# Optimization experiments

Hardware: AMD Instinct MI355X
Metric: run time of the kernel (lower is better)

The kernel has to match this reference:

```python
import jax, jax.numpy as jnp
import numpy as np

# config constants
B, S, H = 4, 2048, 1024
E = 8                 # n_routed_experts
M = 512               # moe_intermediate_size
K = 2                 # num_experts_per_tok
N_SHARED = 2
SM = M * N_SHARED     # shared expert intermediate
G = 64                # gene_size
GE_TEMP = 1.0
ALPHA = 0.001         # aux_loss_alpha
SEQ_AUX = True
NORM_TOPK = True
COS_TEMP = 0.78
CONS_ALPHA = 0.01
LEAKY_SLOPE = 0.01
EPS_COS = 1e-8


def setup_inputs() -> dict:
    key = jax.random.key(0)
    ks = jax.random.split(key, 12)
    sh = 1.0 / np.sqrt(H)
    sm = 1.0 / np.sqrt(M)
    ssm = 1.0 / np.sqrt(SM)
    sg = 1.0 / np.sqrt(G)
    return {
        "hidden_states": jax.random.normal(ks[0], (B, S, H), jnp.float32),
        "g": jax.random.normal(ks[1], (B, G), jnp.float32),
        "wt": jax.random.uniform(ks[2], (E, H), jnp.float32, -sh, sh),   # gate weight_token
        "wg": jax.random.uniform(ks[3], (E, G), jnp.float32, -sg, sg),   # gate weight_gene
        "w_gate": jax.random.uniform(ks[4], (E, H, M), jnp.float32, -sh, sh),
        "w_up": jax.random.uniform(ks[5], (E, H, M), jnp.float32, -sh, sh),
        "w_down": jax.random.uniform(ks[6], (E, M, H), jnp.float32, -sm, sm),
        "sw_gate": jax.random.uniform(ks[7], (H, SM), jnp.float32, -sh, sh),
        "sw_up": jax.random.uniform(ks[8], (H, SM), jnp.float32, -sh, sh),
        "sw_down": jax.random.uniform(ks[9], (SM, H), jnp.float32, -ssm, ssm),
    }


def _leaky(x):
    return jnp.where(x >= 0, x, LEAKY_SLOPE * x)


def _moe_forward(hidden_states, g, wt, wg, w_gate, w_up, w_down, sw_gate, sw_up, sw_down):
    b, s, h = hidden_states.shape
    x = hidden_states.reshape(-1, h)                    # [T, H], T = b*s
    T = x.shape[0]

    # ---- gate ----
    logits_h = x @ wt.T                                 # [T, E]
    logits_g = g @ wg.T                                 # [b, E]
    logits_g = jnp.repeat(logits_g, s, axis=0)          # [T, E]
    logits = (logits_h + logits_g / GE_TEMP) / (1.0 + 1.0 / GE_TEMP)
    scores = jax.nn.softmax(logits, axis=-1)            # [T, E]
    topk_w, topk_idx = jax.lax.top_k(scores, K)         # [T, K]
    if K > 1 and NORM_TOPK:
        topk_w = topk_w / (topk_w.sum(-1, keepdims=True) + 1e-20)

    # aux loss (seq_aux=True)
    onehot = jax.nn.one_hot(topk_idx.reshape(b, s * K), E, dtype=jnp.float32)  # [b, s*K, E]
    ce = onehot.sum(1) / (s * K / E)                    # [b, E]
    aux_loss = (ce * scores.reshape(b, s, E).mean(1)).sum(1).mean() * ALPHA

    # ---- routed experts: dense stacked compute, then gather ----
    gp = _leaky(jnp.einsum('th,ehm->etm', x, w_gate))   # [E, T, M]
    up = jnp.einsum('th,ehm->etm', x, w_up)
    y_all = jnp.einsum('etm,emh->eth', gp * up, w_down) # [E, T, H]
    y_sel = y_all[topk_idx, jnp.arange(T)[:, None], :]  # [T, K, H]
    y = (y_sel * topk_w[..., None]).sum(1).reshape(b, s, h)

    # ---- shared expert ----
    p = (_leaky(hidden_states @ sw_gate) * (hidden_states @ sw_up)) @ sw_down
    y = y + p

    # consistency cosine loss
    num = jnp.sum(y * p, -1)
    den = jnp.maximum(jnp.linalg.norm(y, axis=-1), EPS_COS) * jnp.maximum(jnp.linalg.norm(p, axis=-1), EPS_COS)
    closs = CONS_ALPHA * jnp.mean((num / den) / (1.0 + COS_TEMP))
    return y, aux_loss + closs


def reference(hidden_states, g, wt, wg, w_gate, w_up, w_down, sw_gate, sw_up, sw_down):
    y, _ = _moe_forward(hidden_states, g, wt, wg, w_gate, w_up, w_down, sw_gate, sw_up, sw_down)
    return y
```

## Files before the change

### kernel.cpp

```cpp
#include <hip/hip_runtime.h>
#include <stdint.h>

#define T_TOK 8192
#define H_DIM 1024
#define M_DIM 512
#define SM_DIM 1024
#define E_NUM 8
#define S_SEQ 2048
#define G_DIM 64
#define NASSIGN 16384
#define NSLOT (NASSIGN + E_NUM * 256)
#define MAX_TILES (NASSIGN / 256 + E_NUM)
#define NBLK_PLACE (NASSIGN / 256)

typedef float f32x4 __attribute__((ext_vector_type(4)));
typedef short bf16x8 __attribute__((ext_vector_type(8)));

struct TileDesc { int base; int expert; int nrows; };

#define WAITCNT_VM6 asm volatile("s_waitcnt vmcnt(6)" ::: "memory")
#define WAITCNT_VM4 asm volatile("s_waitcnt vmcnt(4)" ::: "memory")
#define WAITCNT_VM2 asm volatile("s_waitcnt vmcnt(2)" ::: "memory")
#define WAITCNT_VM0 asm volatile("s_waitcnt vmcnt(0)" ::: "memory")
#define WAITCNT_LGKM0 asm volatile("s_waitcnt lgkmcnt(0)" ::: "memory")

static __device__ __forceinline__ ushort f2b(float f) {
  union { float f; uint32_t u; } a; a.f = f;
  uint32_t r = a.u + 0x7fffu + ((a.u >> 16) & 1u);
  return (ushort)(r >> 16);
}
static __device__ __forceinline__ float b2f(ushort u) {
  union { uint32_t u; float f; } a; a.u = ((uint32_t)u) << 16;
  return a.f;
}
static __device__ __forceinline__ int imin(int a, int b) { return a < b ? a : b; }

static __device__ __forceinline__ void gll16(const void* g, void* l) {
  __builtin_amdgcn_global_load_lds(
      (const __attribute__((address_space(1))) void*)g,
      (__attribute__((address_space(3))) void*)l, 16, 0, 0);
}
static __device__ __forceinline__ int xcd_remap(int wg, int nwg) {
  return (wg & 7) * (nwg >> 3) + (wg >> 3);
}

__global__ void cvt_x_kernel(const float* __restrict__ x, ushort* __restrict__ xb) {
  int i = blockIdx.x * 256 + threadIdx.x;
  const float4 v = ((const float4*)x)[i];
  ushort4 o;
  o.x = f2b(v.x); o.y = f2b(v.y); o.z = f2b(v.z); o.w = f2b(v.w);
  ((ushort4*)xb)[i] = o;
}

__global__ void tcvt_kernel(const float* __restrict__ src, ushort* __restrict__ dst, int R, int C) {
  __shared__ float tile[32][33];
  size_t bo = (size_t)blockIdx.z * R * C;
  src += bo; dst += bo;
  int c0 = blockIdx.x * 32, r0 = blockIdx.y * 32;
#pragma unroll
  for (int i = 0; i < 4; ++i)
    tile[threadIdx.y + i * 8][threadIdx.x] =
        src[(size_t)(r0 + threadIdx.y + i * 8) * C + c0 + threadIdx.x];
  __syncthreads();
#pragma unroll
  for (int i = 0; i < 4; ++i)
    dst[(size_t)(c0 + threadIdx.y + i * 8) * R + r0 + threadIdx.x] =
        f2b(tile[threadIdx.x][threadIdx.y + i * 8]);
}

__global__ void lg_kernel(const float* __restrict__ g, const float* __restrict__ wg,
                          float* __restrict__ lg) {
  int tid = threadIdx.x;
  if (tid < 4 * E_NUM) {
    int b = tid >> 3, e = tid & 7;
    float s = 0.f;
    for (int i = 0; i < G_DIM; ++i) s += g[b * G_DIM + i] * wg[e * G_DIM + i];
    lg[tid] = s;
  }
}

__global__ __launch_bounds__(64) void router_kernel(
    const float* __restrict__ x, const float* __restrict__ wt, const float* __restrict__ lg,
    int* __restrict__ tidx, float* __restrict__ tw) {
  int t = blockIdx.x;
  int lane = threadIdx.x;
  const float* xr = x + (size_t)t * H_DIM;
  float a[E_NUM];
#pragma unroll
  for (int e = 0; e < E_NUM; ++e) a[e] = 0.f;
  for (int i = lane; i < H_DIM; i += 64) {
    float xv = xr[i];
#pragma unroll
    for (int e = 0; e < E_NUM; ++e) a[e] += xv * wt[e * H_DIM + i];
  }
#pragma unroll
  for (int e = 0; e < E_NUM; ++e)
    for (int off = 32; off; off >>= 1) a[e] += __shfl_xor(a[e], off, 64);
  if (lane == 0) {
    int b = t / S_SEQ;
    float l[E_NUM];
#pragma unroll
    for (int e = 0; e < E_NUM; ++e) l[e] = 0.5f * (a[e] + lg[b * E_NUM + e]);
    int i1 = 0; float b1 = l[0];
#pragma unroll
    for (int e = 1; e < E_NUM; ++e) if (l[e] > b1) { b1 = l[e]; i1 = e; }
    int i2 = -1; float b2 = -1e30f;
#pragma unroll
    for (int e = 0; e < E_NUM; ++e) if (e != i1 && l[e] > b2) { b2 = l[e]; i2 = e; }
    float e2 = expf(b2 - b1);
    float inv = 1.f / (1.f + e2);
    tidx[t * 2] = i1; tidx[t * 2 + 1] = i2;
    tw[t * 2] = inv;  tw[t * 2 + 1] = e2 * inv;
  }
}

__global__ __launch_bounds__(256) void hist_kernel(const int* __restrict__ tidx,
                                                   int* __restrict__ bcount) {
  __shared__ int h[E_NUM];
  int tid = threadIdx.x;
  if (tid < E_NUM) h[tid] = 0;
  __syncthreads();
  atomicAdd(&h[tidx[blockIdx.x * 256 + tid]], 1);
  __syncthreads();
  if (tid < E_NUM) bcount[blockIdx.x * E_NUM + tid] = h[tid];
}

__global__ __launch_bounds__(64) void scan2_kernel(
    const int* __restrict__ bcount, int* __restrict__ boffs, int* __restrict__ offs,
    TileDesc* __restrict__ desc, int* __restrict__ ndesc) {
  __shared__ int cnt[E_NUM];
  __shared__ int off_s[E_NUM];
  int lane = threadIdx.x;
  if (lane < E_NUM) {
    int s = 0;
    for (int b = 0; b < NBLK_PLACE; ++b) s += bcount[b * E_NUM + lane];
    cnt[lane] = s;
  }
  __syncthreads();
  if (lane == 0) {
    int o = 0, nd = 0;
    for (int e = 0; e < E_NUM; ++e) {
      off_s[e] = o;
      offs[e] = o;
      int n = cnt[e];
      for (int tb = 0; tb < n; tb += 256) {
        desc[nd].base = o + tb; desc[nd].expert = e;
        desc[nd].nrows = imin(n - tb, 256);
        ++nd;
      }
      o += n;
    }
    offs[E_NUM] = o;
    *ndesc = nd;
  }
  __syncthreads();
  if (lane < E_NUM) {
    int run = off_s[lane];
    for (int b = 0; b < NBLK_PLACE; ++b) {
      boffs[b * E_NUM + lane] = run;
      run += bcount[b * E_NUM + lane];
    }
  }
}

__global__ __launch_bounds__(256) void place2_kernel(
    const int* __restrict__ tidx, const int* __restrict__ boffs,
    int* __restrict__ perm, int* __restrict__ slot_of) {
  __shared__ int wcnt[4][E_NUM];
  int tid = threadIdx.x, wv = tid >> 6, lane = tid & 63;
  int i = blockIdx.x * 256 + tid;
  int e = tidx[i];
  unsigned long long lower = (lane == 63) ? 0x7fffffffffffffffull : ((1ull << lane) - 1ull);
  int rank = 0;
#pragma unroll
  for (int ee = 0; ee < E_NUM; ++ee) {
    unsigned long long m = __ballot(e == ee);
    if (e == ee) rank = __popcll(m & lower);
    if (lane == 0) wcnt[wv][ee] = __popcll(m);
  }
  __syncthreads();
  int off = boffs[blockIdx.x * E_NUM + e];
  for (int w = 0; w < wv; ++w) off += wcnt[w][e];
  int pos = off + rank;
  perm[pos] = i >> 1;
  slot_of[i] = pos;
}

template <int DUAL>
static __device__ __forceinline__ void gemm_core8(
    const ushort* __restrict__ A, const ushort* __restrict__ B0,
    const ushort* __restrict__ B1, void* __restrict__ Out, int outf32,
    int Kd, int NdOut, int rowbase, int nrows, int n0,
    const int* __restrict__ perm, ushort* __restrict__ LDS) {
  int tid = threadIdx.x, wv = tid >> 6, lane = tid & 63;
  int wr = wv >> 2, wc = wv & 3;
  int lr = lane & 15, cg = lane >> 4;
  int sid = lane >> 3, dch = lane & 7;

  const ushort* apA[2][2];
  const ushort* apB[2][2];
#pragma unroll
  for (int qm = 0; qm < 2; ++qm)
#pragma unroll
    for (int k = 0; k < 2; ++k) {
      int idx = k * 64 + wv * 8 + sid;
      int gch = dch ^ (idx & 7);
      int grow = (idx >> 6) * 128 + qm * 64 + (idx & 63);
      grow = imin(grow, nrows - 1);
      int arow = perm ? perm[rowbase + grow] : rowbase + grow;
      apA[qm][k] = A + (size_t)arow * Kd + gch * 8;
    }
#pragma unroll
  for (int qn = 0; qn < 2; ++qn)
#pragma unroll
    for (int k = 0; k < 2; ++k) {
      int idx = k * 64 + wv * 8 + sid;
      int gch = dch ^ (idx & 7);
      int vrow = n0 + (idx >> 5) * 64 + qn * 32 + (idx & 31);
      const ushort* src; int brow;
      if (DUAL) {
        src = ((vrow >> 4) & 1) ? B1 : B0;
        brow = (vrow >> 5) * 16 + (vrow & 15);
      } else {
        src = B0; brow = vrow;
      }
      apB[qn][k] = src + (size_t)brow * Kd + gch * 8;
    }

  auto stgA = [&](int qm, int k, int nd) {
    gll16(apA[qm][k], LDS + nd * 16384 + qm * 8192 + (k * 512 + wv * 64) * 8);
    apA[qm][k] += 64;
  };
  auto stgB = [&](int qn, int k, int nd) {
    gll16(apB[qn][k], LDS + 32768 + nd * 16384 + qn * 8192 + (k * 512 + wv * 64) * 8);
    apB[qn][k] += 64;
  };
  auto rdA = [&](int d, int qm, int m, int kk) -> bf16x8 {
    int idx = wr * 64 + m * 16 + lr;
    int ch = (kk * 4 + cg) ^ (idx & 7);
    return *(const bf16x8*)(LDS + d * 16384 + qm * 8192 + idx * 64 + ch * 8);
  };
  auto rdB = [&](int d, int qn, int n, int kk) -> bf16x8 {
    int idx = wc * 32 + n * 16 + lr;
    int ch = (kk * 4 + cg) ^ (idx & 7);
    return *(const bf16x8*)(LDS + 32768 + d * 16384 + qn * 8192 + idx * 64 + ch * 8);
  };

  f32x4 acc[2][2][4][2];
#pragma unroll
  for (int qm = 0; qm < 2; ++qm)
#pragma unroll
    for (int qn = 0; qn < 2; ++qn)
#pragma unroll
      for (int m = 0; m < 4; ++m)
#pragma unroll
        for (int n = 0; n < 2; ++n) acc[qm][qn][m][n] = (f32x4){0.f, 0.f, 0.f, 0.f};

  int nk = Kd >> 6;
  stgA(0, 0, 0); stgA(0, 1, 0);
  stgB(0, 0, 0); stgB(0, 1, 0);
  stgB(1, 0, 0); stgB(1, 1, 0);
  stgA(1, 0, 0); stgA(1, 1, 0);
  WAITCNT_VM4;
  __builtin_amdgcn_s_barrier();

  for (int t = 0; t < nk; ++t) {
    int cur = t & 1, nxt = cur ^ 1;
    bool hn = (t + 1 < nk);
    bf16x8 a0f[4][2], a1f[4][2], b0f[2][2], b1f[2][2];

#pragma unroll
    for (int m = 0; m < 4; ++m) { a0f[m][0] = rdA(cur, 0, m, 0); a0f[m][1] = rdA(cur, 0, m, 1); }
#pragma unroll
    for (int n = 0; n < 2; ++n) { b0f[n][0] = rdB(cur, 0, n, 0); b0f[n][1] = rdB(cur, 0, n, 1); }
    if (hn) { stgA(0, 0, nxt); stgA(0, 1, nxt); WAITCNT_VM4; } else { WAITCNT_VM2; }
    WAITCNT_LGKM0;
    __builtin_amdgcn_s_barrier();
    __builtin_amdgcn_s_setprio(1);
#pragma unroll
    for (int m = 0; m < 4; ++m)
#pragma unroll
      for (int n = 0; n < 2; ++n) {
        acc[0][0][m][n] = __builtin_amdgcn_mfma_f32_16x16x32_bf16(a0f[m][0], b0f[n][0], acc[0][0][m][n], 0, 0, 0);
        acc[0][0][m][n] = __builtin_amdgcn_mfma_f32_16x16x32_bf16(a0f[m][1], b0f[n][1], acc[0][0][m][n], 0, 0, 0);
      }
    __builtin_amdgcn_s_setprio(0);

#pragma unroll
    for (int n = 0; n < 2; ++n) { b1f[n][0] = rdB(cur, 1, n, 0); b1f[n][1] = rdB(cur, 1, n, 1); }
    if (hn) { stgB(0, 0, nxt); stgB(0, 1, nxt); WAITCNT_VM4; } else { WAITCNT_VM0; }
    WAITCNT_LGKM0;
    __builtin_amdgcn_s_barrier();
    __builtin_amdgcn_s_setprio(1);
#pragma unroll
    for (int m = 0; m < 4; ++m)
#pragma unroll
      for (int n = 0; n < 2; ++n) {
        acc[0][1][m][n] = __builtin_amdgcn_mfma_f32_16x16x32_bf16(a0f[m][0], b1f[n][0], acc[0][1][m][n], 0, 0, 0);
        acc[0][1][m][n] = __builtin_amdgcn_mfma_f32_16x16x32_bf16(a0f[m][1], b1f[n][1], acc[0][1][m][n], 0, 0, 0);
      }
    __builtin_amdgcn_s_setprio(0);

#pragma unroll
    for (int m = 0; m < 4; ++m) { a1f[m][0] = rdA(cur, 1, m, 0); a1f[m][1] = rdA(cur, 1, m, 1); }
    if (hn) { stgB(1, 0, nxt); stgB(1, 1, nxt); WAITCNT_VM6; }
    WAITCNT_LGKM0;
    __builtin_amdgcn_s_barrier();
    __builtin_amdgcn_s_setprio(1);
#pragma unroll
    for (int m = 0; m < 4; ++m)
#pragma unroll
      for (int n = 0; n < 2; ++n) {
        acc[1][0][m][n] = __builtin_amdgcn_mfma_f32_16x16x32_bf16(a1f[m][0], b0f[n][0], acc[1][0][m][n], 0, 0, 0);
        acc[1][0][m][n] = __builtin_amdgcn_mfma_f32_16x16x32_bf16(a1f[m][1], b0f[n][1], acc[1][0][m][n], 0, 0, 0);
      }
    __builtin_amdgcn_s_setprio(0);

    if (hn) { stgA(1, 0, nxt); stgA(1, 1, nxt); WAITCNT_VM4; }
    WAITCNT_LGKM0;
    __builtin_amdgcn_s_barrier();
    __builtin_amdgcn_s_setprio(1);
#pragma unroll
    for (int m = 0; m < 4; ++m)
#pragma unroll
      for (int n = 0; n < 2; ++n) {
        acc[1][1][m][n] = __builtin_amdgcn_mfma_f32_16x16x32_bf16(a1f[m][0], b1f[n][0], acc[1][1][m][n], 0, 0, 0);
        acc[1][1][m][n] = __builtin_amdgcn_mfma_f32_16x16x32_bf16(a1f[m][1], b1f[n][1], acc[1][1][m][n], 0, 0, 0);
      }
    __builtin_amdgcn_s_setprio(0);
  }

#pragma unroll
  for (int qm = 0; qm < 2; ++qm)
#pragma unroll
    for (int qn = 0; qn < 2; ++qn)
#pragma unroll
      for (int m = 0; m < 4; ++m)
#pragma unroll
        for (int r = 0; r < 4; ++r) {
          int row = wr * 128 + qm * 64 + m * 16 + cg * 4 + r;
          if (row < nrows) {
            if (DUAL) {
              float gv = acc[qm][qn][m][0][r], uv = acc[qm][qn][m][1][r];
              float hv = (gv >= 0.f ? gv : 0.01f * gv) * uv;
              int col = ((n0 >> 5) + wc * 2 + qn) * 16 + lr;
              ((ushort*)Out)[(size_t)(rowbase + row) * NdOut + col] = f2b(hv);
            } else {
#pragma unroll
              for (int n = 0; n < 2; ++n) {
                int col = n0 + wc * 64 + qn * 32 + n * 16 + lr;
                size_t o = (size_t)(rowbase + row) * NdOut + col;
                if (outf32) ((float*)Out)[o] = acc[qm][qn][m][n][r];
                else ((ushort*)Out)[o] = f2b(acc[qm][qn][m][n][r]);
              }
            }
          }
        }
}

__global__ __launch_bounds__(512) void gemm_dual_all(
    const ushort* __restrict__ xb, const ushort* __restrict__ swg,
    const ushort* __restrict__ swu, ushort* __restrict__ hsh,
    const ushort* __restrict__ wg, const ushort* __restrict__ wu,
    ushort* __restrict__ h_e, const int* __restrict__ perm,
    const TileDesc* __restrict__ desc, const int* __restrict__ ndesc) {
  __shared__ ushort LDS[65536];
  int id = xcd_remap(blockIdx.x, gridDim.x);
  if (id < 256) {
    int mt = id >> 3, n0 = (id & 7) * 256;
    gemm_core8<1>(xb, swg, swu, hsh, 0, H_DIM, SM_DIM, mt * 256, 256, n0, nullptr, LDS);
  } else {
    int rid = id - 256;
    int mt = rid >> 2, n0 = (rid & 3) * 256;
    if (mt >= *ndesc) return;
    TileDesc d = desc[mt];
    size_t wo = (size_t)d.expert * M_DIM * H_DIM;
    gemm_core8<1>(xb, wg + wo, wu + wo, h_e, 0, H_DIM, M_DIM, d.base, d.nrows, n0, perm, LDS);
  }
}

__global__ __launch_bounds__(512) void gemm_down_all(
    const ushort* __restrict__ hsh, const ushort* __restrict__ swd, float* __restrict__ y,
    const ushort* __restrict__ h_e, const ushort* __restrict__ wd, ushort* __restrict__ ye,
    const TileDesc* __restrict__ desc, const int* __restrict__ ndesc) {
  __shared__ ushort LDS[65536];
  int id = xcd_remap(blockIdx.x, gridDim.x);
  if (id < 128) {
    int mt = id >> 2, n0 = (id & 3) * 256;
    gemm_core8<0>(hsh, swd, nullptr, (void*)y, 1, SM_DIM, H_DIM, mt * 256, 256, n0, nullptr, LDS);
  } else {
    int rid = id - 128;
    int mt = rid >> 2, n0 = (rid & 3) * 256;
    if (mt >= *ndesc) return;
    TileDesc d = desc[mt];
    gemm_core8<0>(h_e, wd + (size_t)d.expert * H_DIM * M_DIM, nullptr, (void*)ye, 0,
                  M_DIM, H_DIM, d.base, d.nrows, n0, nullptr, LDS);
  }
}

__global__ void final_kernel(float* __restrict__ y, const ushort* __restrict__ ye,
                             const int* __restrict__ slot_of, const float* __restrict__ tw) {
  int i = blockIdx.x * 256 + threadIdx.x;
  int t = i >> 8;
  int c4 = (i & 255) * 4;
  int s0 = slot_of[t * 2], s1 = slot_of[t * 2 + 1];
  float w0 = tw[t * 2], w1 = tw[t * 2 + 1];
  float4 v = ((float4*)y)[i];
  ushort4 a = *(const ushort4*)(ye + (size_t)s0 * H_DIM + c4);
  ushort4 b = *(const ushort4*)(ye + (size_t)s1 * H_DIM + c4);
  v.x += w0 * b2f(a.x) + w1 * b2f(b.x);
  v.y += w0 * b2f(a.y) + w1 * b2f(b.y);
  v.z += w0 * b2f(a.z) + w1 * b2f(b.z);
  v.w += w0 * b2f(a.w) + w1 * b2f(b.w);
  ((float4*)y)[i] = v;
}

extern "C" void kernel_launch(void* const* d_in, const int* in_sizes, int n_in,
                              void* d_out, int out_size, void* d_ws, size_t ws_size,
                              hipStream_t stream) {
  const float* x       = (const float*)d_in[0];
  const float* g       = (const float*)d_in[1];
  const float* wt      = (const float*)d_in[2];
  const float* wg      = (const float*)d_in[3];
  const float* w_gate  = (const float*)d_in[4];
  const float* w_up    = (const float*)d_in[5];
  const float* w_down  = (const float*)d_in[6];
  const float* sw_gate = (const float*)d_in[7];
  const float* sw_up   = (const float*)d_in[8];
  const float* sw_down = (const float*)d_in[9];
  float* y = (float*)d_out;

  char* p = (char*)d_ws;
  auto alloc = [&](size_t bytes) -> char* {
    char* r = p;
    p += (bytes + 255) & ~(size_t)255;
    return r;
  };
  ushort* xb    = (ushort*)alloc((size_t)T_TOK * H_DIM * 2);
  ushort* wg_t  = (ushort*)alloc((size_t)E_NUM * M_DIM * H_DIM * 2);
  ushort* wu_t  = (ushort*)alloc((size_t)E_NUM * M_DIM * H_DIM * 2);
  ushort* wd_t  = (ushort*)alloc((size_t)E_NUM * H_DIM * M_DIM * 2);
  ushort* swg_t = (ushort*)alloc((size_t)SM_DIM * H_DIM * 2);
  ushort* swu_t = (ushort*)alloc((size_t)SM_DIM * H_DIM * 2);
  ushort* swd_t = (ushort*)alloc((size_t)H_DIM * SM_DIM * 2);
  float* lg     = (float*)alloc(4 * E_NUM * 4);
  int* tidx     = (int*)alloc(NASSIGN * 4);
  float* tw     = (float*)alloc(NASSIGN * 4);
  int* bcount   = (int*)alloc(NBLK_PLACE * E_NUM * 4);
  int* boffs    = (int*)alloc(NBLK_PLACE * E_NUM * 4);
  int* offs     = (int*)alloc((E_NUM + 1) * 4);
  int* ndesc    = (int*)alloc(4);
  int* perm     = (int*)alloc(NASSIGN * 4);
  int* slot_of  = (int*)alloc(NASSIGN * 4);
  TileDesc* desc = (TileDesc*)alloc(MAX_TILES * sizeof(TileDesc));
  ushort* h_e   = (ushort*)alloc((size_t)NSLOT * M_DIM * 2);
  ushort* hsh   = (ushort*)alloc((size_t)T_TOK * SM_DIM * 2);
  ushort* ye    = (ushort*)alloc((size_t)NSLOT * H_DIM * 2);
  (void)ws_size; (void)in_sizes; (void)n_in; (void)out_size;

  cvt_x_kernel<<<T_TOK * H_DIM / 4 / 256, 256, 0, stream>>>(x, xb);
  dim3 tb(32, 8);
  tcvt_kernel<<<dim3(M_DIM / 32, H_DIM / 32, E_NUM), tb, 0, stream>>>(w_gate, wg_t, H_DIM, M_DIM);
  tcvt_kernel<<<dim3(M_DIM / 32, H_DIM / 32, E_NUM), tb, 0, stream>>>(w_up, wu_t, H_DIM, M_DIM);
  tcvt_kernel<<<dim3(H_DIM / 32, M_DIM / 32, E_NUM), tb, 0, stream>>>(w_down, wd_t, M_DIM, H_DIM);
  tcvt_kernel<<<dim3(SM_DIM / 32, H_DIM / 32, 1), tb, 0, stream>>>(sw_gate, swg_t, H_DIM, SM_DIM);
  tcvt_kernel<<<dim3(SM_DIM / 32, H_DIM / 32, 1), tb, 0, stream>>>(sw_up, swu_t, H_DIM, SM_DIM);
  tcvt_kernel<<<dim3(H_DIM / 32, SM_DIM / 32, 1), tb, 0, stream>>>(sw_down, swd_t, SM_DIM, H_DIM);

  lg_kernel<<<1, 32, 0, stream>>>(g, wg, lg);
  router_kernel<<<T_TOK, 64, 0, stream>>>(x, wt, lg, tidx, tw);
  hist_kernel<<<NBLK_PLACE, 256, 0, stream>>>(tidx, bcount);
  scan2_kernel<<<1, 64, 0, stream>>>(bcount, boffs, offs, desc, ndesc);
  place2_kernel<<<NBLK_PLACE, 256, 0, stream>>>(tidx, boffs, perm, slot_of);

  gemm_dual_all<<<256 + MAX_TILES * 4, 512, 0, stream>>>(
      xb, swg_t, swu_t, hsh, wg_t, wu_t, h_e, perm, desc, ndesc);
  gemm_down_all<<<128 + MAX_TILES * 4, 512, 0, stream>>>(
      hsh, swd_t, y, h_e, wd_t, ye, desc, ndesc);

  final_kernel<<<T_TOK * H_DIM / 4 / 256, 256, 0, stream>>>(y, ye, slot_of, tw);
}
```

Baseline: 222.2 us.

## Switch GEMM core to 32x32 MFMA and fuse conversion and routing launches

The GEMM core moves from 16x16x32 to 32x32x16 bf16 MFMA instructions, with new LDS fragment indexing, accumulator layout and epilogue mapping. For the dual GEMM, gate and up weights are now staged as two separate 128-row halves instead of interleaved 16-row groups. The six weight transpose-convert launches are merged into one kernel, and the x-to-bf16 conversion and gene logits are folded into the router kernel, cutting launch count and one full read of x. The larger MFMA shape reduces LDS fragment reads per FLOP, but the new index mapping risks bank conflicts or layout mismatches.

```diff
diff --git a/kernel.cpp b/kernel.cpp
--- a/kernel.cpp
+++ b/kernel.cpp
@@ -14,6 +14,7 @@
 #define NBLK_PLACE (NASSIGN / 256)
 
 typedef float f32x4 __attribute__((ext_vector_type(4)));
+typedef float f32x16 __attribute__((ext_vector_type(16)));
 typedef short bf16x8 __attribute__((ext_vector_type(8)));
 
 struct TileDesc { int base; int expert; int nrows; };
@@ -44,19 +45,27 @@
   return (wg & 7) * (nwg >> 3) + (wg >> 3);
 }
 
-__global__ void cvt_x_kernel(const float* __restrict__ x, ushort* __restrict__ xb) {
-  int i = blockIdx.x * 256 + threadIdx.x;
-  const float4 v = ((const float4*)x)[i];
-  ushort4 o;
-  o.x = f2b(v.x); o.y = f2b(v.y); o.z = f2b(v.z); o.w = f2b(v.w);
-  ((ushort4*)xb)[i] = o;
-}
-
-__global__ void tcvt_kernel(const float* __restrict__ src, ushort* __restrict__ dst, int R, int C) {
+__global__ void wcvt_kernel(const float* __restrict__ w_gate, const float* __restrict__ w_up,
+                            const float* __restrict__ w_down, const float* __restrict__ sw_gate,
+                            const float* __restrict__ sw_up, const float* __restrict__ sw_down,
+                            ushort* __restrict__ wg_t, ushort* __restrict__ wu_t,
+                            ushort* __restrict__ wd_t, ushort* __restrict__ swg_t,
+                            ushort* __restrict__ swu_t, ushort* __restrict__ swd_t) {
   __shared__ float tile[32][33];
-  size_t bo = (size_t)blockIdx.z * R * C;
+  int id = blockIdx.x;
+  const float* src; ushort* dst; int R, C, t;
+  if (id < 4096)        { src = w_gate;  dst = wg_t;  R = 1024; C = 512;  t = id; }
+  else if (id < 8192)   { src = w_up;    dst = wu_t;  R = 1024; C = 512;  t = id - 4096; }
+  else if (id < 12288)  { src = w_down;  dst = wd_t;  R = 512;  C = 1024; t = id - 8192; }
+  else if (id < 13312)  { src = sw_gate; dst = swg_t; R = 1024; C = 1024; t = id - 12288; }
+  else if (id < 14336)  { src = sw_up;   dst = swu_t; R = 1024; C = 1024; t = id - 13312; }
+  else                  { src = sw_down; dst = swd_t; R = 1024; C = 1024; t = id - 14336; }
+  int tc = C >> 5;
+  int tpm = (R >> 5) * tc;
+  int e = t / tpm, tt = t % tpm;
+  int c0 = (tt % tc) * 32, r0 = (tt / tc) * 32;
+  size_t bo = (size_t)e * R * C;
   src += bo; dst += bo;
-  int c0 = blockIdx.x * 32, r0 = blockIdx.y * 32;
 #pragma unroll
   for (int i = 0; i < 4; ++i)
     tile[threadIdx.y + i * 8][threadIdx.x] =
@@ -68,39 +77,43 @@
         f2b(tile[threadIdx.x][threadIdx.y + i * 8]);
 }
 
-__global__ void lg_kernel(const float* __restrict__ g, const float* __restrict__ wg,
-                          float* __restrict__ lg) {
-  int tid = threadIdx.x;
-  if (tid < 4 * E_NUM) {
-    int b = tid >> 3, e = tid & 7;
-    float s = 0.f;
-    for (int i = 0; i < G_DIM; ++i) s += g[b * G_DIM + i] * wg[e * G_DIM + i];
-    lg[tid] = s;
-  }
-}
-
 __global__ __launch_bounds__(64) void router_kernel(
-    const float* __restrict__ x, const float* __restrict__ wt, const float* __restrict__ lg,
+    const float* __restrict__ x, const float* __restrict__ wt, const float* __restrict__ g,
+    const float* __restrict__ wgm, ushort* __restrict__ xb,
     int* __restrict__ tidx, float* __restrict__ tw) {
   int t = blockIdx.x;
   int lane = threadIdx.x;
-  const float* xr = x + (size_t)t * H_DIM;
+  const float4* xr4 = (const float4*)x + (size_t)t * 256;
+  ushort4* xb4 = (ushort4*)xb + (size_t)t * 256;
   float a[E_NUM];
 #pragma unroll
   for (int e = 0; e < E_NUM; ++e) a[e] = 0.f;
-  for (int i = lane; i < H_DIM; i += 64) {
-    float xv = xr[i];
-#pragma unroll
-    for (int e = 0; e < E_NUM; ++e) a[e] += xv * wt[e * H_DIM + i];
+#pragma unroll
+  for (int j = 0; j < 4; ++j) {
+    float4 v = xr4[lane + 64 * j];
+    ushort4 o;
+    o.x = f2b(v.x); o.y = f2b(v.y); o.z = f2b(v.z); o.w = f2b(v.w);
+    xb4[lane + 64 * j] = o;
+#pragma unroll
+    for (int e = 0; e < E_NUM; ++e) {
+      float4 wv = ((const float4*)(wt + (size_t)e * H_DIM))[lane + 64 * j];
+      a[e] += v.x * wv.x + v.y * wv.y + v.z * wv.z + v.w * wv.w;
+    }
   }
 #pragma unroll
   for (int e = 0; e < E_NUM; ++e)
     for (int off = 32; off; off >>= 1) a[e] += __shfl_xor(a[e], off, 64);
+  float lge = 0.f;
+  int b = t / S_SEQ;
+  if (lane < E_NUM) {
+    const float* gv = g + b * G_DIM;
+    const float* wv = wgm + lane * G_DIM;
+    for (int i = 0; i < G_DIM; ++i) lge += gv[i] * wv[i];
+  }
+  float l[E_NUM];
+#pragma unroll
+  for (int e = 0; e < E_NUM; ++e) l[e] = 0.5f * (a[e] + __shfl(lge, e, 64));
   if (lane == 0) {
-    int b = t / S_SEQ;
-    float l[E_NUM];
-#pragma unroll
-    for (int e = 0; e < E_NUM; ++e) l[e] = 0.5f * (a[e] + lg[b * E_NUM + e]);
     int i1 = 0; float b1 = l[0];
 #pragma unroll
     for (int e = 1; e < E_NUM; ++e) if (l[e] > b1) { b1 = l[e]; i1 = e; }
@@ -194,7 +207,7 @@
     const int* __restrict__ perm, ushort* __restrict__ LDS) {
   int tid = threadIdx.x, wv = tid >> 6, lane = tid & 63;
   int wr = wv >> 2, wc = wv & 3;
-  int lr = lane & 15, cg = lane >> 4;
+  int l31 = lane & 31, hi = lane >> 5;
   int sid = lane >> 3, dch = lane & 7;
 
   const ushort* apA[2][2];
@@ -211,50 +224,48 @@
       apA[qm][k] = A + (size_t)arow * Kd + gch * 8;
     }
 #pragma unroll
-  for (int qn = 0; qn < 2; ++qn)
+  for (int n = 0; n < 2; ++n)
 #pragma unroll
     for (int k = 0; k < 2; ++k) {
       int idx = k * 64 + wv * 8 + sid;
       int gch = dch ^ (idx & 7);
-      int vrow = n0 + (idx >> 5) * 64 + qn * 32 + (idx & 31);
       const ushort* src; int brow;
       if (DUAL) {
-        src = ((vrow >> 4) & 1) ? B1 : B0;
-        brow = (vrow >> 5) * 16 + (vrow & 15);
+        src = n ? B1 : B0;
+        brow = (n0 >> 1) + idx;
       } else {
-        src = B0; brow = vrow;
+        src = B0;
+        brow = n0 + n * 128 + idx;
       }
-      apB[qn][k] = src + (size_t)brow * Kd + gch * 8;
+      apB[n][k] = src + (size_t)brow * Kd + gch * 8;
     }
 
   auto stgA = [&](int qm, int k, int nd) {
     gll16(apA[qm][k], LDS + nd * 16384 + qm * 8192 + (k * 512 + wv * 64) * 8);
     apA[qm][k] += 64;
   };
-  auto stgB = [&](int qn, int k, int nd) {
-    gll16(apB[qn][k], LDS + 32768 + nd * 16384 + qn * 8192 + (k * 512 + wv * 64) * 8);
-    apB[qn][k] += 64;
+  auto stgB = [&](int n, int k, int nd) {
+    gll16(apB[n][k], LDS + 32768 + nd * 16384 + n * 8192 + (k * 512 + wv * 64) * 8);
+    apB[n][k] += 64;
   };
-  auto rdA = [&](int d, int qm, int m, int kk) -> bf16x8 {
-    int idx = wr * 64 + m * 16 + lr;
-    int ch = (kk * 4 + cg) ^ (idx & 7);
+  auto rdA = [&](int d, int qm, int m, int ks) -> bf16x8 {
+    int idx = wr * 64 + m * 32 + l31;
+    int ch = (ks * 2 + hi) ^ (idx & 7);
     return *(const bf16x8*)(LDS + d * 16384 + qm * 8192 + idx * 64 + ch * 8);
   };
-  auto rdB = [&](int d, int qn, int n, int kk) -> bf16x8 {
-    int idx = wc * 32 + n * 16 + lr;
-    int ch = (kk * 4 + cg) ^ (idx & 7);
-    return *(const bf16x8*)(LDS + 32768 + d * 16384 + qn * 8192 + idx * 64 + ch * 8);
+  auto rdB = [&](int d, int n, int ks) -> bf16x8 {
+    int idx = wc * 32 + l31;
+    int ch = (ks * 2 + hi) ^ (idx & 7);
+    return *(const bf16x8*)(LDS + 32768 + d * 16384 + n * 8192 + idx * 64 + ch * 8);
   };
 
-  f32x4 acc[2][2][4][2];
+  f32x16 acc[2][2][2];
 #pragma unroll
   for (int qm = 0; qm < 2; ++qm)
 #pragma unroll
-    for (int qn = 0; qn < 2; ++qn)
-#pragma unroll
-      for (int m = 0; m < 4; ++m)
-#pragma unroll
-        for (int n = 0; n < 2; ++n) acc[qm][qn][m][n] = (f32x4){0.f, 0.f, 0.f, 0.f};
+    for (int m = 0; m < 2; ++m)
+#pragma unroll
+      for (int n = 0; n < 2; ++n) acc[qm][m][n] = (f32x16)(0.f);
 
   int nk = Kd >> 6;
   stgA(0, 0, 0); stgA(0, 1, 0);
@@ -267,53 +278,51 @@
   for (int t = 0; t < nk; ++t) {
     int cur = t & 1, nxt = cur ^ 1;
     bool hn = (t + 1 < nk);
-    bf16x8 a0f[4][2], a1f[4][2], b0f[2][2], b1f[2][2];
-
-#pragma unroll
-    for (int m = 0; m < 4; ++m) { a0f[m][0] = rdA(cur, 0, m, 0); a0f[m][1] = rdA(cur, 0, m, 1); }
-#pragma unroll
-    for (int n = 0; n < 2; ++n) { b0f[n][0] = rdB(cur, 0, n, 0); b0f[n][1] = rdB(cur, 0, n, 1); }
+    bf16x8 a0f[2][4], a1f[2][4], b0f[4], b1f[4];
+
+#pragma unroll
+    for (int m = 0; m < 2; ++m)
+#pragma unroll
+      for (int ks = 0; ks < 4; ++ks) a0f[m][ks] = rdA(cur, 0, m, ks);
+#pragma unroll
+    for (int ks = 0; ks < 4; ++ks) b0f[ks] = rdB(cur, 0, ks);
     if (hn) { stgA(0, 0, nxt); stgA(0, 1, nxt); WAITCNT_VM4; } else { WAITCNT_VM2; }
     WAITCNT_LGKM0;
     __builtin_amdgcn_s_barrier();
     __builtin_amdgcn_s_setprio(1);
 #pragma unroll
-    for (int m = 0; m < 4; ++m)
-#pragma unroll
-      for (int n = 0; n < 2; ++n) {
-        acc[0][0][m][n] = __builtin_amdgcn_mfma_f32_16x16x32_bf16(a0f[m][0], b0f[n][0], acc[0][0][m][n], 0, 0, 0);
-        acc[0][0][m][n] = __builtin_amdgcn_mfma_f32_16x16x32_bf16(a0f[m][1], b0f[n][1], acc[0][0][m][n], 0, 0, 0);
-      }
+    for (int m = 0; m < 2; ++m)
+#pragma unroll
+      for (int ks = 0; ks < 4; ++ks)
+        acc[0][m][0] = __builtin_amdgcn_mfma_f32_32x32x16_bf16(a0f[m][ks], b0f[ks], acc[0][m][0], 0, 0, 0);
     __builtin_amdgcn_s_setprio(0);
 
 #pragma unroll
-    for (int n = 0; n < 2; ++n) { b1f[n][0] = rdB(cur, 1, n, 0); b1f[n][1] = rdB(cur, 1, n, 1); }
+    for (int ks = 0; ks < 4; ++ks) b1f[ks] = rdB(cur, 1, ks);
     if (hn) { stgB(0, 0, nxt); stgB(0, 1, nxt); WAITCNT_VM4; } else { WAITCNT_VM0; }
     WAITCNT_LGKM0;
     __builtin_amdgcn_s_barrier();
     __builtin_amdgcn_s_setprio(1);
 #pragma unroll
-    for (int m = 0; m < 4; ++m)
-#pragma unroll
-      for (int n = 0; n < 2; ++n) {
-        acc[0][1][m][n] = __builtin_amdgcn_mfma_f32_16x16x32_bf16(a0f[m][0], b1f[n][0], acc[0][1][m][n], 0, 0, 0);
-        acc[0][1][m][n] = __builtin_amdgcn_mfma_f32_16x16x32_bf16(a0f[m][1], b1f[n][1], acc[0][1][m][n], 0, 0, 0);
-      }
+    for (int m = 0; m < 2; ++m)
+#pragma unroll
+      for (int ks = 0; ks < 4; ++ks)
+        acc[0][m][1] = __builtin_amdgcn_mfma_f32_32x32x16_bf16(a0f[m][ks], b1f[ks], acc[0][m][1], 0, 0, 0);
     __builtin_amdgcn_s_setprio(0);
 
 #pragma unroll
-    for (int m = 0; m < 4; ++m) { a1f[m][0] = rdA(cur, 1, m, 0); a1f[m][1] = rdA(cur, 1, m, 1); }
+    for (int m = 0; m < 2; ++m)
+#pragma unroll
+      for (int ks = 0; ks < 4; ++ks) a1f[m][ks] = rdA(cur, 1, m, ks);
     if (hn) { stgB(1, 0, nxt); stgB(1, 1, nxt); WAITCNT_VM6; }
     WAITCNT_LGKM0;
     __builtin_amdgcn_s_barrier();
     __builtin_amdgcn_s_setprio(1);
 #pragma unroll
-    for (int m = 0; m < 4; ++m)
-#pragma unroll
-      for (int n = 0; n < 2; ++n) {
-        acc[1][0][m][n] = __builtin_amdgcn_mfma_f32_16x16x32_bf16(a1f[m][0], b0f[n][0], acc[1][0][m][n], 0, 0, 0);
-        acc[1][0][m][n] = __builtin_amdgcn_mfma_f32_16x16x32_bf16(a1f[m][1], b0f[n][1], acc[1][0][m][n], 0, 0, 0);
-      }
+    for (int m = 0; m < 2; ++m)
+#pragma unroll
+      for (int ks = 0; ks < 4; ++ks)
+        acc[1][m][0] = __builtin_amdgcn_mfma_f32_32x32x16_bf16(a1f[m][ks], b0f[ks], acc[1][m][0], 0, 0, 0);
     __builtin_amdgcn_s_setprio(0);
 
     if (hn) { stgA(1, 0, nxt); stgA(1, 1, nxt); WAITCNT_VM4; }
@@ -321,37 +330,36 @@
     __builtin_amdgcn_s_barrier();
     __builtin_amdgcn_s_setprio(1);
 #pragma unroll
-    for (int m = 0; m < 4; ++m)
-#pragma unroll
-      for (int n = 0; n < 2; ++n) {
-        acc[1][1][m][n] = __builtin_amdgcn_mfma_f32_16x16x32_bf16(a1f[m][0], b1f[n][0], acc[1][1][m][n], 0, 0, 0);
-        acc[1][1][m][n] = __builtin_amdgcn_mfma_f32_16x16x32_bf16(a1f[m][1], b1f[n][1], acc[1][1][m][n], 0, 0, 0);
-      }
+    for (int m = 0; m < 2; ++m)
+#pragma unroll
+      for (int ks = 0; ks < 4; ++ks)
+        acc[1][m][1] = __builtin_amdgcn_mfma_f32_32x32x16_bf16(a1f[m][ks], b1f[ks], acc[1][m][1], 0, 0, 0);
     __builtin_amdgcn_s_setprio(0);
   }
 
+  int rq = hi * 4;
 #pragma unroll
   for (int qm = 0; qm < 2; ++qm)
 #pragma unroll
-    for (int qn = 0; qn < 2; ++qn)
-#pragma unroll
-      for (int m = 0; m < 4; ++m)
+    for (int m = 0; m < 2; ++m)
+#pragma unroll
+      for (int c = 0; c < 4; ++c)
 #pragma unroll
         for (int r = 0; r < 4; ++r) {
-          int row = wr * 128 + qm * 64 + m * 16 + cg * 4 + r;
+          int row = wr * 128 + qm * 64 + m * 32 + c * 8 + r + rq;
           if (row < nrows) {
             if (DUAL) {
-              float gv = acc[qm][qn][m][0][r], uv = acc[qm][qn][m][1][r];
+              float gv = acc[qm][m][0][c * 4 + r], uv = acc[qm][m][1][c * 4 + r];
               float hv = (gv >= 0.f ? gv : 0.01f * gv) * uv;
-              int col = ((n0 >> 5) + wc * 2 + qn) * 16 + lr;
+              int col = (n0 >> 1) + wc * 32 + l31;
               ((ushort*)Out)[(size_t)(rowbase + row) * NdOut + col] = f2b(hv);
             } else {
 #pragma unroll
               for (int n = 0; n < 2; ++n) {
-                int col = n0 + wc * 64 + qn * 32 + n * 16 + lr;
+                int col = n0 + n * 128 + wc * 32 + l31;
                 size_t o = (size_t)(rowbase + row) * NdOut + col;
-                if (outf32) ((float*)Out)[o] = acc[qm][qn][m][n][r];
-                else ((ushort*)Out)[o] = f2b(acc[qm][qn][m][n][r]);
+                if (outf32) ((float*)Out)[o] = acc[qm][m][n][c * 4 + r];
+                else ((ushort*)Out)[o] = f2b(acc[qm][m][n][c * 4 + r]);
               }
             }
           }
@@ -443,7 +451,6 @@
   ushort* swg_t = (ushort*)alloc((size_t)SM_DIM * H_DIM * 2);
   ushort* swu_t = (ushort*)alloc((size_t)SM_DIM * H_DIM * 2);
   ushort* swd_t = (ushort*)alloc((size_t)H_DIM * SM_DIM * 2);
-  float* lg     = (float*)alloc(4 * E_NUM * 4);
   int* tidx     = (int*)alloc(NASSIGN * 4);
   float* tw     = (float*)alloc(NASSIGN * 4);
   int* bcount   = (int*)alloc(NBLK_PLACE * E_NUM * 4);
@@ -458,17 +465,10 @@
   ushort* ye    = (ushort*)alloc((size_t)NSLOT * H_DIM * 2);
   (void)ws_size; (void)in_sizes; (void)n_in; (void)out_size;
 
-  cvt_x_kernel<<<T_TOK * H_DIM / 4 / 256, 256, 0, stream>>>(x, xb);
   dim3 tb(32, 8);
-  tcvt_kernel<<<dim3(M_DIM / 32, H_DIM / 32, E_NUM), tb, 0, stream>>>(w_gate, wg_t, H_DIM, M_DIM);
-  tcvt_kernel<<<dim3(M_DIM / 32, H_DIM / 32, E_NUM), tb, 0, stream>>>(w_up, wu_t, H_DIM, M_DIM);
-  tcvt_kernel<<<dim3(H_DIM / 32, M_DIM / 32, E_NUM), tb, 0, stream>>>(w_down, wd_t, M_DIM, H_DIM);
-  tcvt_kernel<<<dim3(SM_DIM / 32, H_DIM / 32, 1), tb, 0, stream>>>(sw_gate, swg_t, H_DIM, SM_DIM);
-  tcvt_kernel<<<dim3(SM_DIM / 32, H_DIM / 32, 1), tb, 0, stream>>>(sw_up, swu_t, H_DIM, SM_DIM);
-  tcvt_kernel<<<dim3(H_DIM / 32, SM_DIM / 32, 1), tb, 0, stream>>>(sw_down, swd_t, SM_DIM, H_DIM);
-
-  lg_kernel<<<1, 32, 0, stream>>>(g, wg, lg);
-  router_kernel<<<T_TOK, 64, 0, stream>>>(x, wt, lg, tidx, tw);
+  wcvt_kernel<<<15360, tb, 0, stream>>>(w_gate, w_up, w_down, sw_gate, sw_up, sw_down,
+                                        wg_t, wu_t, wd_t, swg_t, swu_t, swd_t);
+  router_kernel<<<T_TOK, 64, 0, stream>>>(x, wt, g, wg, xb, tidx, tw);
   hist_kernel<<<NBLK_PLACE, 256, 0, stream>>>(tidx, bcount);
   scan2_kernel<<<1, 64, 0, stream>>>(bcount, boffs, offs, desc, ndesc);
   place2_kernel<<<NBLK_PLACE, 256, 0, stream>>>(tidx, boffs, perm, slot_of);
```

Result: no change. 223.5 us (+0.6%).
